# Kernel optimization log

Hardware: AMD Instinct MI355X
Metric: run time of the kernel (lower is better)

Reference implementation:

```python
import jax, jax.numpy as jnp
import numpy as np

EPS = 1e-12  # matches torch F.normalize default eps
TEMP = 0.1


def _gram(x):
    # L2-normalize rows; for unit vectors 1 - 0.5*||xi-xj||^2 == xi . xj
    n = x / jnp.maximum(jnp.linalg.norm(x, axis=-1, keepdims=True), EPS)
    return n @ n.T  # [N, N]


def setup_inputs() -> dict:
    key = jax.random.key(0)
    k1, k2, k3, k4 = jax.random.split(key, 4)
    N, D = 4096, 512
    return {
        "fm_rgb": jax.random.normal(k1, (N, D), dtype=jnp.float32),
        "fm_depth": jax.random.normal(k2, (N, D), dtype=jnp.float32),
        "fm_ir": jax.random.normal(k3, (N, D), dtype=jnp.float32),
        "fm_t": jax.random.normal(k4, (N, D), dtype=jnp.float32),
    }


def reference(fm_rgb, fm_depth, fm_ir, fm_t):
    G_rgb = _gram(fm_rgb)
    G_depth = _gram(fm_depth)
    G_ir = _gram(fm_ir)
    G_t = _gram(fm_t)
    inv_t = 1.0 / TEMP
    loss_rgb = jnp.mean((G_t * inv_t - G_rgb * inv_t) ** 2)
    loss_depth = jnp.mean((G_t * inv_t - G_depth * inv_t) ** 2)
    loss_ir = jnp.mean((G_t * inv_t - G_ir * inv_t) ** 2)
    return loss_rgb + loss_depth + loss_ir
```

## Files before the change

### kernel.cpp

```cpp
#include <hip/hip_runtime.h>
#include <hip/hip_bf16.h>


typedef __attribute__((ext_vector_type(4))) float floatx4;
typedef __attribute__((ext_vector_type(2))) long long llx2;
typedef __attribute__((ext_vector_type(8))) int intx8;

#define N_ROWS 4096
#define DDIM   512
#define LOSS_SCALE 9.094947017729282e-11f

__device__ __forceinline__ const float* sel_mod(int mod, const float* a,
                                                const float* b, const float* c,
                                                const float* d) {
  return mod == 0 ? a : mod == 1 ? b : mod == 2 ? c : d;
}

__device__ __forceinline__ float bfr(float x) {
  __hip_bfloat16 h = __float2bfloat16(x);
  unsigned short u = *(unsigned short*)&h;
  return __uint_as_float(((unsigned int)u) << 16);
}

__global__ __launch_bounds__(512) void preprocess_kernel(
    const float* __restrict__ in0, const float* __restrict__ in1,
    const float* __restrict__ in2, const float* __restrict__ in3,
    unsigned char* __restrict__ nT8, float* __restrict__ out) {
  int mod = blockIdx.y;
  int k0 = blockIdx.x * 64;
  const float* X = sel_mod(mod, in0, in1, in2, in3) + (size_t)k0 * DDIM;

  if (blockIdx.x == 0 && blockIdx.y == 0 && threadIdx.x == 0)
    out[0] = 0.f;

  __shared__ float rsc[64];
  __shared__ unsigned int t8[512 * 17];

  int t = threadIdx.x;
  int a = t >> 5;
  int bg = t & 31;

  float4 v[4][4];
#pragma unroll
  for (int q = 0; q < 4; ++q)
#pragma unroll
    for (int p = 0; p < 4; ++p)
      v[q][p] = ((const float4*)(X + (size_t)(4 * a + q) * DDIM + p * 128))[bg];

  float ss[4];
#pragma unroll
  for (int q = 0; q < 4; ++q) {
    float acc = 0.f;
#pragma unroll
    for (int p = 0; p < 4; ++p) {
      float4 u = v[q][p];
      acc += u.x * u.x + u.y * u.y + u.z * u.z + u.w * u.w;
    }
    ss[q] = acc;
  }
#pragma unroll
  for (int off = 16; off > 0; off >>= 1)
#pragma unroll
    for (int q = 0; q < 4; ++q) ss[q] += __shfl_down(ss[q], off, 32);
  if (bg == 0) {
#pragma unroll
    for (int q = 0; q < 4; ++q)
      rsc[4 * a + q] = 16.0f / fmaxf(sqrtf(ss[q]), 1e-12f);
  }
  __syncthreads();

  float sc[4];
#pragma unroll
  for (int q = 0; q < 4; ++q) sc[q] = rsc[4 * a + q];

#pragma unroll
  for (int p = 0; p < 4; ++p)
#pragma unroll
    for (int j = 0; j < 4; ++j) {
      float f0 = bfr(((const float*)&v[0][p])[j] * sc[0]);
      float f1 = bfr(((const float*)&v[1][p])[j] * sc[1]);
      float f2 = bfr(((const float*)&v[2][p])[j] * sc[2]);
      float f3 = bfr(((const float*)&v[3][p])[j] * sc[3]);
      unsigned int pk = __builtin_amdgcn_cvt_pk_fp8_f32(f0, f1, 0, 0);
      pk = __builtin_amdgcn_cvt_pk_fp8_f32(f2, f3, pk, 1);
      t8[(p * 128 + bg * 4 + j) * 17 + a] = pk;
    }
  __syncthreads();

#pragma unroll
  for (int it = 0; it < 4; ++it) {
    int idx = it * 512 + t;
    int col = idx >> 2;
    int g = idx & 3;
    uint4 o;
    o.x = t8[col * 17 + g * 4 + 0];
    o.y = t8[col * 17 + g * 4 + 1];
    o.z = t8[col * 17 + g * 4 + 2];
    o.w = t8[col * 17 + g * 4 + 3];
    *(uint4*)(nT8 + ((size_t)(mod * DDIM + col)) * N_ROWS + k0 + g * 16) = o;
  }
}

__device__ __forceinline__ void stage_half(
    const unsigned char* __restrict__ base, int k0, unsigned char* ls,
    int lane) {
  int rr = lane >> 3;
  int s = lane & 7;
#pragma unroll
  for (int c = 0; c < 8; ++c) {
    int row = c * 8 + rr;
    int gc = s ^ ((row >> 1) & 7);
    const unsigned char* g = base + (size_t)row * N_ROWS + k0 + gc * 16;
    __builtin_amdgcn_global_load_lds(
        (__attribute__((address_space(1))) void*)(void*)g,
        (__attribute__((address_space(3))) void*)(void*)&ls[c * 1024],
        16, 0, 0);
  }
}

__device__ __forceinline__ void compute_w(const unsigned char* ls,
                                          floatx4 acc[4][2], int wn, int lm,
                                          int lq) {
  intx8 A8[4], B8[2];
#pragma unroll
  for (int mi = 0; mi < 4; ++mi) {
    int row = mi * 16 + lm;
    int sw = (row >> 1) & 7;
    *(llx2*)&A8[mi] = *(const llx2*)&ls[row * 128 + ((lq * 2) ^ sw) * 16];
    *((llx2*)&A8[mi] + 1) =
        *(const llx2*)&ls[row * 128 + ((lq * 2 + 1) ^ sw) * 16];
  }
#pragma unroll
  for (int ni = 0; ni < 2; ++ni) {
    int row = wn + ni * 16 + lm;
    int sw = (row >> 1) & 7;
    *(llx2*)&B8[ni] =
        *(const llx2*)&ls[8192 + row * 128 + ((lq * 2) ^ sw) * 16];
    *((llx2*)&B8[ni] + 1) =
        *(const llx2*)&ls[8192 + row * 128 + ((lq * 2 + 1) ^ sw) * 16];
  }
  __builtin_amdgcn_s_setprio(1);
#pragma unroll
  for (int mi = 0; mi < 4; ++mi)
#pragma unroll
    for (int ni = 0; ni < 2; ++ni)
      acc[mi][ni] = __builtin_amdgcn_mfma_scale_f32_16x16x128_f8f6f4(
          A8[mi], B8[ni], acc[mi][ni], 0, 0,
          0, 0x7F, 0, 0x7F);
  __builtin_amdgcn_s_setprio(0);
}

__global__ __launch_bounds__(128) void gram_frob_kernel(
    const unsigned char* __restrict__ nT8, float* __restrict__ out) {
  __shared__ __align__(16) unsigned char ls[4][16384];
  __shared__ float red[2];

  int bx = blockIdx.x;
  int job = (bx & 7) * 42 + (bx >> 3);

  int pa_, pb_, ti, tj;
  float wgt;
  if (job < 144) {
    int p = job / 36;
    int t36 = job - p * 36;
    int i = 0;
    while (t36 >= 8 - i) { t36 -= 8 - i; ++i; }
    ti = i;
    tj = i + t36;
    const int   sm[4] = {3, 0, 1, 2};
    const float sw_[4] = {3.f, 1.f, 1.f, 1.f};
    pa_ = sm[p];
    pb_ = sm[p];
    wgt = sw_[p] * (ti == tj ? 1.f : 2.f);
  } else {
    int r = job - 144;
    int p = r >> 6;
    int t64 = r & 63;
    ti = t64 >> 3;
    tj = t64 & 7;
    pa_ = 3;
    pb_ = p;
    wgt = -2.f;
  }

  const unsigned char* Abase = nT8 + ((size_t)pa_ * DDIM + ti * 64) * N_ROWS;
  const unsigned char* Bbase = nT8 + ((size_t)pb_ * DDIM + tj * 64) * N_ROWS;

  int t = threadIdx.x;
  int w = t >> 6;
  int lane = t & 63;
  int lm = lane & 15;
  int lq = lane >> 4;
  int wn = w * 32;
  const unsigned char* sbase = (w == 0) ? Abase : Bbase;
  int soff = w * 8192;

  floatx4 zero = {0.f, 0.f, 0.f, 0.f};
  floatx4 acc[4][2];
#pragma unroll
  for (int mi = 0; mi < 4; ++mi)
#pragma unroll
    for (int ni = 0; ni < 2; ++ni) acc[mi][ni] = zero;

  stage_half(sbase, 0, ls[0] + soff, lane);
  stage_half(sbase, 128, ls[1] + soff, lane);
  stage_half(sbase, 256, ls[2] + soff, lane);
  for (int i = 0; i < 29; ++i) {
    asm volatile("s_waitcnt vmcnt(16)" ::: "memory");
    __builtin_amdgcn_sched_barrier(0);
    __builtin_amdgcn_s_barrier();
    stage_half(sbase, (i + 3) * 128, ls[(i + 3) & 3] + soff, lane);
    compute_w(ls[i & 3], acc, wn, lm, lq);
  }
  asm volatile("s_waitcnt vmcnt(16)" ::: "memory");
  __builtin_amdgcn_sched_barrier(0);
  __builtin_amdgcn_s_barrier();
  compute_w(ls[1], acc, wn, lm, lq);
  asm volatile("s_waitcnt vmcnt(8)" ::: "memory");
  __builtin_amdgcn_sched_barrier(0);
  __builtin_amdgcn_s_barrier();
  compute_w(ls[2], acc, wn, lm, lq);
  asm volatile("s_waitcnt vmcnt(0)" ::: "memory");
  __builtin_amdgcn_sched_barrier(0);
  __builtin_amdgcn_s_barrier();
  compute_w(ls[3], acc, wn, lm, lq);

  float s = 0.f;
#pragma unroll
  for (int mi = 0; mi < 4; ++mi)
#pragma unroll
    for (int ni = 0; ni < 2; ++ni)
#pragma unroll
      for (int r = 0; r < 4; ++r) {
        float v = acc[mi][ni][r];
        s += v * v;
      }
#pragma unroll
  for (int off = 32; off > 0; off >>= 1) s += __shfl_down(s, off, 64);
  if (lane == 0) red[w] = s;
  __syncthreads();
  if (t == 0)
    atomicAdd(out, wgt * LOSS_SCALE * (red[0] + red[1]));
}

extern "C" void kernel_launch(void* const* d_in, const int* in_sizes, int n_in,
                              void* d_out, int out_size, void* d_ws, size_t ws_size,
                              hipStream_t stream) {
  const float* in_rgb   = (const float*)d_in[0];
  const float* in_depth = (const float*)d_in[1];
  const float* in_ir    = (const float*)d_in[2];
  const float* in_t     = (const float*)d_in[3];

  unsigned char* nT8 = (unsigned char*)d_ws;

  preprocess_kernel<<<dim3(64, 4), 512, 0, stream>>>(
      in_rgb, in_depth, in_ir, in_t, nT8, (float*)d_out);
  gram_frob_kernel<<<dim3(336), 128, 0, stream>>>(nT8, (float*)d_out);
}
```

Measured before the change: 105.2 us.

## Block fp8 transposed layout, reorder jobs by tile pair, deepen LDS pipeline

Preprocess now writes the normalized fp8 data in a blocked layout: 64-column chunks by 64-row k-blocks. Each tile stage becomes contiguous 64-byte segments instead of strided 4096-byte rows. The gram kernel's job mapping groups all seven modality jobs that share the same (ti,tj) tile pair so they land together, which should help L2 reuse. The mixed products are split into two mirrored halves. The LDS ring goes from 4 to 5 buffers with one more stage in flight. The final reduction drops the shared-memory sync and has each wave issue its own atomic, which doubles the atomic count but removes a barrier.

```diff
diff --git a/kernel.cpp b/kernel.cpp
--- a/kernel.cpp
+++ b/kernel.cpp
@@ -87,6 +87,7 @@
     }
   __syncthreads();
 
+  size_t rbase = (size_t)(mod * 64 + blockIdx.x) * 32768;
 #pragma unroll
   for (int it = 0; it < 4; ++it) {
     int idx = it * 512 + t;
@@ -97,20 +98,23 @@
     o.y = t8[col * 17 + g * 4 + 1];
     o.z = t8[col * 17 + g * 4 + 2];
     o.w = t8[col * 17 + g * 4 + 3];
-    *(uint4*)(nT8 + ((size_t)(mod * DDIM + col)) * N_ROWS + k0 + g * 16) = o;
+    *(uint4*)(nT8 + rbase + (size_t)idx * 16) = o;
   }
 }
 
 __device__ __forceinline__ void stage_half(
-    const unsigned char* __restrict__ base, int k0, unsigned char* ls,
-    int lane) {
+    const unsigned char* __restrict__ mbase, int cbase, int k0,
+    unsigned char* ls, int lane) {
   int rr = lane >> 3;
   int s = lane & 7;
+  int kb0 = k0 >> 6;
 #pragma unroll
   for (int c = 0; c < 8; ++c) {
     int row = c * 8 + rr;
     int gc = s ^ ((row >> 1) & 7);
-    const unsigned char* g = base + (size_t)row * N_ROWS + k0 + gc * 16;
+    const unsigned char* g =
+        mbase + ((size_t)(kb0 + (gc >> 2)) * 512 + cbase + row) * 64 +
+        (gc & 3) * 16;
     __builtin_amdgcn_global_load_lds(
         (__attribute__((address_space(1))) void*)(void*)g,
         (__attribute__((address_space(3))) void*)(void*)&ls[c * 1024],
@@ -152,39 +156,47 @@
 
 __global__ __launch_bounds__(128) void gram_frob_kernel(
     const unsigned char* __restrict__ nT8, float* __restrict__ out) {
-  __shared__ __align__(16) unsigned char ls[4][16384];
-  __shared__ float red[2];
+  __shared__ __align__(16) unsigned char ls[5][16384];
 
   int bx = blockIdx.x;
   int job = (bx & 7) * 42 + (bx >> 3);
 
-  int pa_, pb_, ti, tj;
+  int rem = job, ti = 7, tj = 7;
+  for (int i = 0; i < 8; ++i) {
+    int rowlen = 7 + 10 * (7 - i);
+    if (rem < rowlen) {
+      if (rem < 7) {
+        ti = i; tj = i;
+      } else {
+        int r2 = rem - 7;
+        ti = i; tj = i + 1 + r2 / 10;
+        rem = r2 % 10;
+      }
+      break;
+    }
+    rem -= rowlen;
+  }
+
+  int pa_, pb_, a0, b0;
   float wgt;
-  if (job < 144) {
-    int p = job / 36;
-    int t36 = job - p * 36;
-    int i = 0;
-    while (t36 >= 8 - i) { t36 -= 8 - i; ++i; }
-    ti = i;
-    tj = i + t36;
-    const int   sm[4] = {3, 0, 1, 2};
-    const float sw_[4] = {3.f, 1.f, 1.f, 1.f};
-    pa_ = sm[p];
-    pb_ = sm[p];
-    wgt = sw_[p] * (ti == tj ? 1.f : 2.f);
+  if (ti == tj) {
+    if (rem < 4) { pa_ = pb_ = rem; wgt = (rem == 3) ? 3.f : 1.f; }
+    else         { pa_ = 3; pb_ = rem - 4; wgt = -2.f; }
+    a0 = ti * 64; b0 = ti * 64;
   } else {
-    int r = job - 144;
-    int p = r >> 6;
-    int t64 = r & 63;
-    ti = t64 >> 3;
-    tj = t64 & 7;
-    pa_ = 3;
-    pb_ = p;
-    wgt = -2.f;
-  }
-
-  const unsigned char* Abase = nT8 + ((size_t)pa_ * DDIM + ti * 64) * N_ROWS;
-  const unsigned char* Bbase = nT8 + ((size_t)pb_ * DDIM + tj * 64) * N_ROWS;
+    if (rem < 4) {
+      pa_ = pb_ = rem; wgt = (rem == 3) ? 6.f : 2.f;
+      a0 = ti * 64; b0 = tj * 64;
+    } else {
+      int k = rem - 4;
+      pa_ = 3; pb_ = k >> 1; wgt = -2.f;
+      if (k & 1) { a0 = tj * 64; b0 = ti * 64; }
+      else       { a0 = ti * 64; b0 = tj * 64; }
+    }
+  }
+
+  const unsigned char* Abase = nT8 + (size_t)pa_ * 2097152;
+  const unsigned char* Bbase = nT8 + (size_t)pb_ * 2097152;
 
   int t = threadIdx.x;
   int w = t >> 6;
@@ -192,7 +204,8 @@
   int lm = lane & 15;
   int lq = lane >> 4;
   int wn = w * 32;
-  const unsigned char* sbase = (w == 0) ? Abase : Bbase;
+  const unsigned char* mbase = (w == 0) ? Abase : Bbase;
+  int cb = (w == 0) ? a0 : b0;
   int soff = w * 8192;
 
   floatx4 zero = {0.f, 0.f, 0.f, 0.f};
@@ -202,28 +215,39 @@
 #pragma unroll
     for (int ni = 0; ni < 2; ++ni) acc[mi][ni] = zero;
 
-  stage_half(sbase, 0, ls[0] + soff, lane);
-  stage_half(sbase, 128, ls[1] + soff, lane);
-  stage_half(sbase, 256, ls[2] + soff, lane);
-  for (int i = 0; i < 29; ++i) {
-    asm volatile("s_waitcnt vmcnt(16)" ::: "memory");
+  unsigned char* p0 = ls[0] + soff;
+  unsigned char* p1 = ls[1] + soff;
+  unsigned char* p2 = ls[2] + soff;
+  unsigned char* p3 = ls[3] + soff;
+  unsigned char* p4 = ls[4] + soff;
+  stage_half(mbase, cb, 0, p0, lane);
+  stage_half(mbase, cb, 128, p1, lane);
+  stage_half(mbase, cb, 256, p2, lane);
+  stage_half(mbase, cb, 384, p3, lane);
+  for (int i = 0; i < 28; ++i) {
+    asm volatile("s_waitcnt vmcnt(24)" ::: "memory");
     __builtin_amdgcn_sched_barrier(0);
     __builtin_amdgcn_s_barrier();
-    stage_half(sbase, (i + 3) * 128, ls[(i + 3) & 3] + soff, lane);
-    compute_w(ls[i & 3], acc, wn, lm, lq);
-  }
+    stage_half(mbase, cb, (i + 4) * 128, p4, lane);
+    compute_w(p0 - soff, acc, wn, lm, lq);
+    unsigned char* tmp = p0; p0 = p1; p1 = p2; p2 = p3; p3 = p4; p4 = tmp;
+  }
+  asm volatile("s_waitcnt vmcnt(24)" ::: "memory");
+  __builtin_amdgcn_sched_barrier(0);
+  __builtin_amdgcn_s_barrier();
+  compute_w(p0 - soff, acc, wn, lm, lq);
   asm volatile("s_waitcnt vmcnt(16)" ::: "memory");
   __builtin_amdgcn_sched_barrier(0);
   __builtin_amdgcn_s_barrier();
-  compute_w(ls[1], acc, wn, lm, lq);
+  compute_w(p1 - soff, acc, wn, lm, lq);
   asm volatile("s_waitcnt vmcnt(8)" ::: "memory");
   __builtin_amdgcn_sched_barrier(0);
   __builtin_amdgcn_s_barrier();
-  compute_w(ls[2], acc, wn, lm, lq);
+  compute_w(p2 - soff, acc, wn, lm, lq);
   asm volatile("s_waitcnt vmcnt(0)" ::: "memory");
   __builtin_amdgcn_sched_barrier(0);
   __builtin_amdgcn_s_barrier();
-  compute_w(ls[3], acc, wn, lm, lq);
+  compute_w(p3 - soff, acc, wn, lm, lq);
 
   float s = 0.f;
 #pragma unroll
@@ -237,10 +261,8 @@
       }
 #pragma unroll
   for (int off = 32; off > 0; off >>= 1) s += __shfl_down(s, off, 64);
-  if (lane == 0) red[w] = s;
-  __syncthreads();
-  if (t == 0)
-    atomicAdd(out, wgt * LOSS_SCALE * (red[0] + red[1]));
+  if (lane == 0)
+    atomicAdd(out, wgt * LOSS_SCALE * s);
 }
 
 extern "C" void kernel_launch(void* const* d_in, const int* in_sizes, int n_in,
```

After: 101.8 us. 1.03x faster.
